# Optimization experiments

Hardware: AMD Instinct MI355X
Metric: run time of the kernel (lower is better)

The kernel has to match this reference:

```python
import jax, jax.numpy as jnp
import numpy as np

B, M, D, H, C = 256, 512, 768, 8, 768


def setup_inputs() -> dict:
    key = jax.random.key(0)
    ks = jax.random.split(key, 12)
    rn = lambda k, shp, s=1.0: jax.random.normal(k, shp, dtype=jnp.float32) * s
    w = 1.0 / np.sqrt(D)
    return dict(
        controller_state=rn(ks[0], (B, C)),
        write_data=rn(ks[1], (B, D)),
        memory=rn(ks[2], (M, D), 0.1),
        in_proj_w=rn(ks[3], (3 * D, D), w), in_proj_b=jnp.zeros((3 * D,), jnp.float32),
        out_w=rn(ks[4], (D, D), w), out_b=jnp.zeros((D,), jnp.float32),
        read_w=rn(ks[5], (D, C), w), read_b=jnp.zeros((D,), jnp.float32),
        write_w=rn(ks[6], (D, C), w), write_b=jnp.zeros((D,), jnp.float32),
        erase_w=rn(ks[7], (D, C), w), erase_b=jnp.zeros((D,), jnp.float32),
        ug_w=rn(ks[8], (1, C + D), w), ug_b=jnp.zeros((1,), jnp.float32),
        fg_w=rn(ks[9], (1, C + D), w), fg_b=jnp.zeros((1,), jnp.float32),
    )


def _mha(q, kv, in_proj_w, in_proj_b, out_w, out_b, num_heads):
    # q: [B,1,D] query, kv: [B,M,D] keys=values. Matches torch.nn.MultiheadAttention
    # (batch_first, eval mode -> no dropout, average_attn_weights=True).
    b, m, d = kv.shape
    dh = d // num_heads
    wq, wk, wv = jnp.split(in_proj_w, 3, axis=0)
    bq, bk, bv = jnp.split(in_proj_b, 3, axis=0)
    qh = (q @ wq.T + bq).reshape(b, 1, num_heads, dh).transpose(0, 2, 1, 3)   # [B,H,1,dh]
    kh = (kv @ wk.T + bk).reshape(b, m, num_heads, dh).transpose(0, 2, 1, 3)  # [B,H,M,dh]
    vh = (kv @ wv.T + bv).reshape(b, m, num_heads, dh).transpose(0, 2, 1, 3)
    scores = jnp.einsum('bhqd,bhkd->bhqk', qh, kh) / jnp.sqrt(jnp.float32(dh))
    attn = jax.nn.softmax(scores, axis=-1)                                    # [B,H,1,M]
    ctx = jnp.einsum('bhqk,bhkd->bhqd', attn, vh)
    ctx = ctx.transpose(0, 2, 1, 3).reshape(b, 1, d)
    out = ctx @ out_w.T + out_b
    return out, attn.mean(axis=1)  # out [B,1,D], weights averaged over heads [B,1,M]


def reference(controller_state, write_data, memory, in_proj_w, in_proj_b,
              out_w, out_b, read_w, read_b, write_w, write_b,
              erase_w, erase_b, ug_w, ug_b, fg_w, fg_b):
    b = controller_state.shape[0]
    memory_batch = jnp.broadcast_to(memory[None], (b,) + memory.shape)        # [B,M,D]

    read_key = (controller_state @ read_w.T + read_b)[:, None, :]             # [B,1,D]
    read_data, _ = _mha(read_key, memory_batch, in_proj_w, in_proj_b, out_w, out_b, H)
    read_data = read_data[:, 0, :]                                            # [B,D]

    write_key = (controller_state @ write_w.T + write_b)[:, None, :]
    erase_vec = jax.nn.sigmoid(controller_state @ erase_w.T + erase_b)[:, None, :]  # [B,1,D]
    _, write_weights = _mha(write_key, memory_batch, in_proj_w, in_proj_b, out_w, out_b, H)
    ww = write_weights[:, 0, :]                                               # [B,M]

    combined = jnp.concatenate([controller_state, read_data], axis=-1)        # [B,C+D]
    ug = jax.nn.sigmoid(combined @ ug_w.T + ug_b)                             # [B,1]
    fg = jax.nn.sigmoid(combined @ fg_w.T + fg_b)                             # [B,1]

    erase_term = ww[:, :, None] * erase_vec * fg[:, :, None]                  # [B,M,D]
    write_term = ww[:, :, None] * write_data[:, None, :] * ug[:, :, None]     # [B,M,D]
    updated_memory = memory_batch + (write_term - erase_term)
    return read_data, updated_memory
```

## Files before the change

kernel.cpp:

```cpp
#include <hip/hip_runtime.h>
#include <math.h>

#define B_ 256
#define M_ 512
#define D_ 768
#define H_ 8
#define DH_ 96
#define C_ 768

typedef float  f32x4_t __attribute__((ext_vector_type(4)));
typedef short  s16x8   __attribute__((ext_vector_type(8)));
typedef unsigned short u16;

__device__ __forceinline__ u16 cvt_bf16(float f) {
    union { float f; unsigned int u; } v; v.f = f;
    unsigned int r = (v.u + 0x7FFFu + ((v.u >> 16) & 1u)) >> 16;
    return (u16)r;
}
__device__ __forceinline__ float bf16_f32(u16 h) {
    union { unsigned int u; float f; } v; v.u = ((unsigned int)h) << 16;
    return v.f;
}

#define ACC_INIT {{0,0,0,0},{0,0,0,0},{0,0,0,0},{0,0,0,0}}
#define SCALE_ 0.10206207261596577f

template<int BK>
__device__ __forceinline__ void mm64b(
    const u16* __restrict__ A, int lda, const u16* __restrict__ B, int ldb,
    int ksteps, int bRowClamp, u16* lA, u16* lB, f32x4_t* acc, int nfrag)
{
    constexpr int NL = BK / 32;
    const int t = threadIdx.x;
    const int srow = t >> 2, kq = t & 3;
    const int l = t & 63, w = t >> 6;
    const int brow = srow < bRowClamp ? srow : bRowClamp;

    for (int ks = 0; ks < ksteps; ++ks) {
        s16x8 va[NL], vb[NL];
        #pragma unroll
        for (int c = 0; c < NL; ++c) {
            const int ko = ks * BK + (kq * NL + c) * 8;
            va[c] = *reinterpret_cast<const s16x8*>(A + (size_t)srow * lda + ko);
            vb[c] = *reinterpret_cast<const s16x8*>(B + (size_t)brow * ldb + ko);
        }
        __syncthreads();
        #pragma unroll
        for (int c = 0; c < NL; ++c) {
            const int kb = kq * NL + c;
            *reinterpret_cast<s16x8*>(lA + (kb * 64 + srow) * 8) = va[c];
            *reinterpret_cast<s16x8*>(lB + (kb * 64 + srow) * 8) = vb[c];
        }
        __syncthreads();
        #pragma unroll
        for (int ksub = 0; ksub < NL; ++ksub) {
            const int kb = (l >> 4) + ksub * 4;
            s16x8 af = *reinterpret_cast<const s16x8*>(lA + (kb * 64 + w * 16 + (l & 15)) * 8);
            #pragma unroll
            for (int nb = 0; nb < 4; ++nb) {
                if (nb < nfrag) {
                    s16x8 bf = *reinterpret_cast<const s16x8*>(lB + (kb * 64 + nb * 16 + (l & 15)) * 8);
                    acc[nb] = __builtin_amdgcn_mfma_f32_16x16x32_bf16(af, bf, acc[nb], 0, 0, 0);
                }
            }
        }
    }
}

__device__ __forceinline__ void epilogue_f32(
    const f32x4_t* acc, float* out, int ldo, int m0, int n0,
    const float* bias, int act, int nfrag)
{
    const int t = threadIdx.x, l = t & 63, w = t >> 6;
    const int mbase = m0 + w * 16 + (l >> 4) * 4;
    #pragma unroll
    for (int nb = 0; nb < 4; ++nb) {
        if (nb >= nfrag) break;
        const int col = n0 + nb * 16 + (l & 15);
        const float bv = bias ? bias[col] : 0.0f;
        #pragma unroll
        for (int r = 0; r < 4; ++r) {
            float v = acc[nb][r] + bv;
            if (act) v = 1.0f / (1.0f + expf(-v));
            out[(size_t)(mbase + r) * ldo + col] = v;
        }
    }
}

__device__ __forceinline__ void epilogue_bf16(
    const f32x4_t* acc, u16* out, int ldo, int m0, int n0,
    const float* bias, int nfrag)
{
    const int t = threadIdx.x, l = t & 63, w = t >> 6;
    const int mbase = m0 + w * 16 + (l >> 4) * 4;
    #pragma unroll
    for (int nb = 0; nb < 4; ++nb) {
        if (nb >= nfrag) break;
        const int col = n0 + nb * 16 + (l & 15);
        const float bv = bias ? bias[col] : 0.0f;
        #pragma unroll
        for (int r = 0; r < 4; ++r)
            out[(size_t)(mbase + r) * ldo + col] = cvt_bf16(acc[nb][r] + bv);
    }
}

__global__ __launch_bounds__(256) void conv_kernel(
    const float* __restrict__ mem, const float* __restrict__ cs,
    const float* __restrict__ ipw, const float* __restrict__ rw,
    const float* __restrict__ www, const float* __restrict__ ew,
    const float* __restrict__ outw, const float* __restrict__ outb,
    const float* __restrict__ ugw, const float* __restrict__ ugb,
    const float* __restrict__ fgw, const float* __restrict__ fgb,
    u16* __restrict__ memb, u16* __restrict__ csb, u16* __restrict__ ipwb,
    u16* __restrict__ rwb, u16* __restrict__ wwwb, u16* __restrict__ ewb,
    u16* __restrict__ outwb, float* __restrict__ vg, float* __restrict__ gc)
{
    __shared__ float sred[256];
    const int bid = blockIdx.x, t = threadIdx.x;

    if (bid < 2304) {
        const float* src; u16* dst; int base;
        if      (bid < 192)  { src = mem;  dst = memb;  base = bid; }
        else if (bid < 288)  { src = cs;   dst = csb;   base = bid - 192; }
        else if (bid < 1152) { src = ipw;  dst = ipwb;  base = bid - 288; }
        else if (bid < 1440) { src = rw;   dst = rwb;   base = bid - 1152; }
        else if (bid < 1728) { src = www;  dst = wwwb;  base = bid - 1440; }
        else if (bid < 2016) { src = ew;   dst = ewb;   base = bid - 1728; }
        else                 { src = outw; dst = outwb; base = bid - 2016; }
        const size_t i = ((size_t)base * 256 + t) * 8;
        float4 x = *reinterpret_cast<const float4*>(src + i);
        float4 y = *reinterpret_cast<const float4*>(src + i + 4);
        s16x8 o;
        o[0]=cvt_bf16(x.x); o[1]=cvt_bf16(x.y); o[2]=cvt_bf16(x.z); o[3]=cvt_bf16(x.w);
        o[4]=cvt_bf16(y.x); o[5]=cvt_bf16(y.y); o[6]=cvt_bf16(y.z); o[7]=cvt_bf16(y.w);
        *reinterpret_cast<s16x8*>(dst + i) = o;
    } else {
        const int lid = bid - 2304;
        const int v = lid / 12, kt = lid % 12;
        const float* gw = v == 0 ? ugw : fgw;
        const int c = t & 63, g = t >> 6;
        const int col = kt * 64 + c;
        float acc = 0.f;
        #pragma unroll 4
        for (int i = 0; i < 192; ++i) {
            const int row = g * 192 + i;
            acc += outw[(size_t)row * 768 + col] * gw[768 + row];
        }
        sred[t] = acc;
        __syncthreads();
        if (g == 0)
            vg[v * 768 + col] = sred[c] + sred[64 + c] + sred[128 + c] + sred[192 + c];
        if (kt == 0) {
            __syncthreads();
            float cp = outb[t] * gw[768 + t] + outb[t + 256] * gw[768 + t + 256]
                     + outb[t + 512] * gw[768 + t + 512];
            sred[t] = cp; __syncthreads();
            #pragma unroll
            for (int off = 128; off > 0; off >>= 1) {
                if (t < off) sred[t] += sred[t + off];
                __syncthreads();
            }
            if (t == 0) gc[v] = sred[0] + (v == 0 ? ugb[0] : fgb[0]);
        }
    }
}

__global__ __launch_bounds__(256) void stage1_kernel(
    const u16* __restrict__ memb, const u16* __restrict__ csb,
    const u16* __restrict__ ipwb, const float* __restrict__ ipb,
    const u16* __restrict__ rwb, const float* __restrict__ rb,
    const u16* __restrict__ wwwb, const float* __restrict__ ww_b,
    const u16* __restrict__ ewb, const float* __restrict__ eb,
    u16* __restrict__ khb, u16* __restrict__ vhT,
    u16* __restrict__ rwkeysb, float* __restrict__ erase)
{
    __shared__ u16 lA[8192], lB[8192];
    f32x4_t acc[4] = ACC_INIT;
    const int bid = blockIdx.x;
    if (bid < 192) {
        const int mt = bid / 24, nt = bid % 24;
        mm64b<64>(memb + (size_t)mt * 64 * 768, 768,
                  ipwb + (size_t)768 * 768 + (size_t)nt * 64 * 768, 768,
                  12, 63, lA, lB, acc, 4);
        const int t = threadIdx.x, l = t & 63, w = t >> 6;
        const int mbase = mt * 64 + w * 16 + (l >> 4) * 4;
        if (nt < 12) {
            #pragma unroll
            for (int nb = 0; nb < 4; ++nb) {
                const int col = nt * 64 + nb * 16 + (l & 15);
                const float bv = ipb[768 + col];
                #pragma unroll
                for (int r = 0; r < 4; ++r)
                    khb[(size_t)(mbase + r) * 768 + col] = cvt_bf16(acc[nb][r] + bv);
            }
        } else {
            #pragma unroll
            for (int nb = 0; nb < 4; ++nb) {
                const int cg = (nt - 12) * 64 + nb * 16 + (l & 15);
                const int h = cg / 96, d = cg % 96;
                const float bv = ipb[1536 + cg];
                u16* dst = vhT + ((size_t)h * 96 + d) * 512;
                #pragma unroll
                for (int r = 0; r < 4; ++r)
                    dst[mbase + r] = cvt_bf16(acc[nb][r] + bv);
            }
        }
    } else if (bid < 240) {
        const int lid = bid - 192, mt = lid / 12, nt = lid % 12;
        mm64b<64>(csb + (size_t)mt * 64 * 768, 768, rwb + (size_t)nt * 64 * 768, 768,
                  12, 63, lA, lB, acc, 4);
        epilogue_bf16(acc, rwkeysb, 768, mt * 64, nt * 64, rb, 4);
    } else if (bid < 288) {
        const int lid = bid - 240, mt = lid / 12, nt = lid % 12;
        mm64b<64>(csb + (size_t)mt * 64 * 768, 768, wwwb + (size_t)nt * 64 * 768, 768,
                  12, 63, lA, lB, acc, 4);
        epilogue_bf16(acc, rwkeysb + (size_t)256 * 768, 768, mt * 64, nt * 64, ww_b, 4);
    } else {
        const int lid = bid - 288, mt = lid / 12, nt = lid % 12;
        mm64b<64>(csb + (size_t)mt * 64 * 768, 768, ewb + (size_t)nt * 64 * 768, 768,
                  12, 63, lA, lB, acc, 4);
        epilogue_f32(acc, erase, 768, mt * 64, nt * 64, eb, 1, 4);
    }
}

__global__ __launch_bounds__(256) void stage2_kernel(
    const u16* __restrict__ rwkeysb, const u16* __restrict__ ipwb,
    const float* __restrict__ ipb, u16* __restrict__ qrwb)
{
    __shared__ u16 lA[8192], lB[8192];
    f32x4_t acc[4] = ACC_INIT;
    const int mt = blockIdx.x / 12, nt = blockIdx.x % 12;
    mm64b<64>(rwkeysb + (size_t)mt * 64 * 768, 768, ipwb + (size_t)nt * 64 * 768, 768,
              12, 63, lA, lB, acc, 4);
    epilogue_bf16(acc, qrwb, 768, mt * 64, nt * 64, ipb, 4);
}

__global__ __launch_bounds__(256) void scores_kernel(
    const u16* __restrict__ qrwb, const u16* __restrict__ khb, u16* __restrict__ E)
{
    __shared__ u16 lA[2048], lB[2048];
    f32x4_t acc[4] = ACC_INIT;
    const int h = blockIdx.y;
    const int mt = blockIdx.x >> 3, nt = blockIdx.x & 7;
    mm64b<32>(qrwb + (size_t)mt * 64 * 768 + h * 96, 768,
              khb + (size_t)nt * 64 * 768 + h * 96, 768, 3, 63, lA, lB, acc, 4);
    const int t = threadIdx.x, l = t & 63, w = t >> 6;
    const int mbase = mt * 64 + w * 16 + (l >> 4) * 4;
    #pragma unroll
    for (int nb = 0; nb < 4; ++nb) {
        const int col = nt * 64 + nb * 16 + (l & 15);
        #pragma unroll
        for (int r = 0; r < 4; ++r) {
            const float e = expf(fminf(acc[nb][r] * SCALE_, 30.0f));
            E[((size_t)h * 512 + mbase + r) * 512 + col] = cvt_bf16(e);
        }
    }
}

__global__ __launch_bounds__(256) void pv_kernel(
    const u16* __restrict__ E, const u16* __restrict__ vhT, u16* __restrict__ ctxb)
{
    __shared__ u16 lA[8192], lB[8192];
    __shared__ float rinv[64];
    f32x4_t acc[4] = ACC_INIT;
    const int h = blockIdx.z, mt = blockIdx.x, nt = blockIdx.y;
    const int n0 = nt * 64;
    const int nfrag = nt == 0 ? 4 : 2;
    const int bclamp = nt == 0 ? 63 : 31;

    const u16* A  = E + ((size_t)h * 512 + mt * 64) * 512;
    const u16* Bv = vhT + ((size_t)h * 96 + n0) * 512;

    const int t = threadIdx.x;
    const int srow = t >> 2, kq = t & 3;
    const int l = t & 63, w = t >> 6;
    const int brow = srow < bclamp ? srow : bclamp;

    float rs = 0.f;
    for (int ks = 0; ks < 8; ++ks) {
        s16x8 va[2], vb[2];
        #pragma unroll
        for (int c = 0; c < 2; ++c) {
            const int ko = ks * 64 + (kq * 2 + c) * 8;
            va[c] = *reinterpret_cast<const s16x8*>(A + (size_t)srow * 512 + ko);
            vb[c] = *reinterpret_cast<const s16x8*>(Bv + (size_t)brow * 512 + ko);
        }
        #pragma unroll
        for (int c = 0; c < 2; ++c)
            #pragma unroll
            for (int j = 0; j < 8; ++j)
                rs += bf16_f32((u16)va[c][j]);
        __syncthreads();
        #pragma unroll
        for (int c = 0; c < 2; ++c) {
            const int kb = kq * 2 + c;
            *reinterpret_cast<s16x8*>(lA + (kb * 64 + srow) * 8) = va[c];
            *reinterpret_cast<s16x8*>(lB + (kb * 64 + srow) * 8) = vb[c];
        }
        __syncthreads();
        #pragma unroll
        for (int ksub = 0; ksub < 2; ++ksub) {
            const int kb = (l >> 4) + ksub * 4;
            s16x8 af = *reinterpret_cast<const s16x8*>(lA + (kb * 64 + w * 16 + (l & 15)) * 8);
            #pragma unroll
            for (int nb = 0; nb < 4; ++nb) {
                if (nb < nfrag) {
                    s16x8 bf = *reinterpret_cast<const s16x8*>(lB + (kb * 64 + nb * 16 + (l & 15)) * 8);
                    acc[nb] = __builtin_amdgcn_mfma_f32_16x16x32_bf16(af, bf, acc[nb], 0, 0, 0);
                }
            }
        }
    }
    rs += __shfl_xor(rs, 1);
    rs += __shfl_xor(rs, 2);
    if (kq == 0) rinv[srow] = 1.0f / rs;
    __syncthreads();

    const int mbase = w * 16 + (l >> 4) * 4;
    #pragma unroll
    for (int nb = 0; nb < 4; ++nb) {
        if (nb >= nfrag) break;
        const int col = n0 + nb * 16 + (l & 15);
        #pragma unroll
        for (int r = 0; r < 4; ++r) {
            const float v = acc[nb][r] * rinv[mbase + r];
            ctxb[(size_t)(mt * 64 + mbase + r) * 768 + h * 96 + col] = cvt_bf16(v);
        }
    }
}

__global__ __launch_bounds__(256) void finalize_kernel(
    const u16* __restrict__ ctxb, const u16* __restrict__ outwb,
    const float* __restrict__ outb, float* __restrict__ rd_out,
    const float* __restrict__ cs, const float* __restrict__ wdta,
    const float* __restrict__ erase,
    const float* __restrict__ ugw, const float* __restrict__ fgw,
    const float* __restrict__ vg, const float* __restrict__ gc,
    const u16* __restrict__ E,
    float* __restrict__ delta, float* __restrict__ wwb)
{
    __shared__ u16 lA[8192], lB[8192];
    const int bid = blockIdx.x, t = threadIdx.x;
    if (bid < 48) {
        f32x4_t acc[4] = ACC_INIT;
        const int mt = bid / 12, nt = bid % 12;
        mm64b<64>(ctxb + (size_t)mt * 64 * 768, 768, outwb + (size_t)nt * 64 * 768, 768,
                  12, 63, lA, lB, acc, 4);
        epilogue_f32(acc, rd_out, 768, mt * 64, nt * 64, outb, 0, 4);
    } else if (bid < 304) {
        const int b = bid - 48;
        __shared__ float red[8];
        float pu = 0.f, pf = 0.f;
        #pragma unroll
        for (int c = 0; c < 3; ++c) {
            const int i = t + c * 256;
            const float cv = cs[(size_t)b * 768 + i];
            const float xv = bf16_f32(ctxb[(size_t)b * 768 + i]);
            pu += cv * ugw[i] + xv * vg[i];
            pf += cv * fgw[i] + xv * vg[768 + i];
        }
        const int w = t >> 6, l = t & 63;
        #pragma unroll
        for (int off = 32; off > 0; off >>= 1) {
            pu += __shfl_xor(pu, off);
            pf += __shfl_xor(pf, off);
        }
        if (l == 0) { red[w] = pu; red[4 + w] = pf; }
        __syncthreads();
        const float ug = 1.0f / (1.0f + expf(-(red[0] + red[1] + red[2] + red[3] + gc[0])));
        const float fg = 1.0f / (1.0f + expf(-(red[4] + red[5] + red[6] + red[7] + gc[1])));
        #pragma unroll
        for (int c = 0; c < 3; ++c) {
            const int i = t + c * 256;
            delta[(size_t)b * 768 + i] = wdta[(size_t)b * 768 + i] * ug
                                       - erase[(size_t)b * 768 + i] * fg;
        }
    } else {
        const int b = bid - 304;
        __shared__ float linv8[8];
        const int w = t >> 6, l = t & 63;
        #pragma unroll
        for (int hh = 0; hh < 2; ++hh) {
            const int h = w * 2 + hh;
            const u16* row = E + ((size_t)h * 512 + 256 + b) * 512;
            float s = 0.f;
            #pragma unroll
            for (int c = 0; c < 8; ++c) s += bf16_f32(row[c * 64 + l]);
            #pragma unroll
            for (int off = 32; off > 0; off >>= 1) s += __shfl_xor(s, off);
            if (l == 0) linv8[h] = 1.0f / s;
        }
        __syncthreads();
        #pragma unroll
        for (int mm_ = 0; mm_ < 2; ++mm_) {
            const int m = t + mm_ * 256;
            float s = 0.f;
            #pragma unroll
            for (int h = 0; h < H_; ++h)
                s += bf16_f32(E[((size_t)h * 512 + 256 + b) * 512 + m]) * linv8[h];
            wwb[(size_t)b * 512 + m] = s * 0.125f;
        }
    }
}

__global__ __launch_bounds__(192) void update_mem(
    const float* __restrict__ mem, const float* __restrict__ ww,
    const float* __restrict__ delta, float* __restrict__ out)
{
    const int blk = blockIdx.x;
    const int b   = blk >> 6;
    const int m0  = (blk & 63) << 3;
    const int t   = threadIdx.x;

    const f32x4_t d4 = *reinterpret_cast<const f32x4_t*>(delta + (size_t)b * D_ + t * 4);
    const f32x4_t* m4 = reinterpret_cast<const f32x4_t*>(mem);
    f32x4_t* o4 = reinterpret_cast<f32x4_t*>(out + (size_t)b * M_ * D_);

    #pragma unroll
    for (int i = 0; i < 8; ++i) {
        const int m = m0 + i;
        const float w = ww[(size_t)b * M_ + m];
        f32x4_t mm = m4[(size_t)m * 192 + t];
        f32x4_t r = mm + w * d4;
        __builtin_nontemporal_store(r, &o4[(size_t)m * 192 + t]);
    }
}

extern "C" void kernel_launch(void* const* d_in, const int* in_sizes, int n_in,
                              void* d_out, int out_size, void* d_ws, size_t ws_size,
                              hipStream_t stream)
{
    const float* cs   = (const float*)d_in[0];
    const float* wdta = (const float*)d_in[1];
    const float* mem  = (const float*)d_in[2];
    const float* ipw  = (const float*)d_in[3];
    const float* ipb  = (const float*)d_in[4];
    const float* outw = (const float*)d_in[5];
    const float* outb = (const float*)d_in[6];
    const float* rw   = (const float*)d_in[7];
    const float* rb   = (const float*)d_in[8];
    const float* ww_w = (const float*)d_in[9];
    const float* ww_b = (const float*)d_in[10];
    const float* ew   = (const float*)d_in[11];
    const float* eb   = (const float*)d_in[12];
    const float* ugw  = (const float*)d_in[13];
    const float* ugb  = (const float*)d_in[14];
    const float* fgw  = (const float*)d_in[15];
    const float* fgb  = (const float*)d_in[16];

    float* rd_out  = (float*)d_out;
    float* mem_out = (float*)d_out + B_ * D_;

    float* S0 = mem_out;
    u16*   memb    = (u16*)(S0 + 0);
    u16*   csb     = (u16*)(S0 + 196608);
    u16*   ipwb    = (u16*)(S0 + 294912);
    u16*   rwb     = (u16*)(S0 + 1179648);
    u16*   wwwb    = (u16*)(S0 + 1474560);
    u16*   ewb     = (u16*)(S0 + 1769472);
    u16*   outwb   = (u16*)(S0 + 2064384);
    u16*   khb     = (u16*)(S0 + 2359296);
    u16*   vhT     = (u16*)(S0 + 2555904);
    u16*   rwkeysb = (u16*)(S0 + 2752512);
    u16*   qrwb    = (u16*)(S0 + 2949120);

    float* ws    = (float*)d_ws;
    float* erase = ws;
    u16*   ctxb  = (u16*)(ws + 196608);
    u16*   E     = (u16*)(ws + 294912);
    float* vg    =        ws + 1343488;
    float* gc    =        ws + 1345024;
    float* delta =        ws + 1345040;
    float* wwb   =        ws + 1541648;

    conv_kernel<<<2328, 256, 0, stream>>>(mem, cs, ipw, rw, ww_w, ew, outw, outb,
                                          ugw, ugb, fgw, fgb,
                                          memb, csb, ipwb, rwb, wwwb, ewb, outwb,
                                          vg, gc);
    stage1_kernel<<<336, 256, 0, stream>>>(memb, csb, ipwb, ipb, rwb, rb, wwwb, ww_b,
                                           ewb, eb, khb, vhT, rwkeysb, erase);
    stage2_kernel<<<96, 256, 0, stream>>>(rwkeysb, ipwb, ipb, qrwb);
    scores_kernel<<<dim3(64, 8), 256, 0, stream>>>(qrwb, khb, E);
    pv_kernel<<<dim3(4, 2, 8), 256, 0, stream>>>(E, vhT, ctxb);
    finalize_kernel<<<560, 256, 0, stream>>>(ctxb, outwb, outb, rd_out,
                                             cs, wdta, erase, ugw, fgw, vg, gc,
                                             E, delta, wwb);
    update_mem<<<B_ * (M_ / 8), 192, 0, stream>>>(mem, wwb, delta, mem_out);
}
```

Before: 149.9 us.

## Fuse all stages into a persistent cooperative megakernel with grid syncs

Replaces the seven separate kernel launches with one cooperative kernel of 512 persistent blocks. Each stage is now a device function, and the stages are separated by grid-wide syncs. The aim is to remove launch gaps and inter-kernel idle time. The memory-update stage is also reworked to loop over 256-thread blocks with 6 float4 items per thread. In exchange, the streaming update runs at a fixed, lower occupancy, and every grid.sync adds barrier cost. If the cooperative launch fails, the code falls back to separate launches.

```diff
diff --git a/kernel.cpp b/kernel.cpp
--- a/kernel.cpp
+++ b/kernel.cpp
@@ -1,5 +1,8 @@
 #include <hip/hip_runtime.h>
+#include <hip/hip_cooperative_groups.h>
 #include <math.h>
+
+namespace cg = cooperative_groups;
 
 #define B_ 256
 #define M_ 512
@@ -24,6 +27,14 @@
 
 #define ACC_INIT {{0,0,0,0},{0,0,0,0},{0,0,0,0},{0,0,0,0}}
 #define SCALE_ 0.10206207261596577f
+
+struct P {
+    const float *cs, *wdta, *mem, *ipw, *ipb, *outw, *outb;
+    const float *rw, *rb, *www_w, *www_b, *ew, *eb, *ugw, *ugb, *fgw, *fgb;
+    u16 *memb, *csb, *ipwb, *rwb, *wwwb, *ewb, *outwb;
+    u16 *khb, *vhT, *rwkeysb, *qrwb, *E, *ctxb;
+    float *erase, *vg, *gc, *delta, *wwb, *rd_out, *mem_out;
+};
 
 template<int BK>
 __device__ __forceinline__ void mm64b(
@@ -104,29 +115,18 @@
     }
 }
 
-__global__ __launch_bounds__(256) void conv_kernel(
-    const float* __restrict__ mem, const float* __restrict__ cs,
-    const float* __restrict__ ipw, const float* __restrict__ rw,
-    const float* __restrict__ www, const float* __restrict__ ew,
-    const float* __restrict__ outw, const float* __restrict__ outb,
-    const float* __restrict__ ugw, const float* __restrict__ ugb,
-    const float* __restrict__ fgw, const float* __restrict__ fgb,
-    u16* __restrict__ memb, u16* __restrict__ csb, u16* __restrict__ ipwb,
-    u16* __restrict__ rwb, u16* __restrict__ wwwb, u16* __restrict__ ewb,
-    u16* __restrict__ outwb, float* __restrict__ vg, float* __restrict__ gc)
-{
-    __shared__ float sred[256];
-    const int bid = blockIdx.x, t = threadIdx.x;
-
+
+__device__ __forceinline__ void conv_body(const P& p, int bid, int t, float* sred)
+{
     if (bid < 2304) {
         const float* src; u16* dst; int base;
-        if      (bid < 192)  { src = mem;  dst = memb;  base = bid; }
-        else if (bid < 288)  { src = cs;   dst = csb;   base = bid - 192; }
-        else if (bid < 1152) { src = ipw;  dst = ipwb;  base = bid - 288; }
-        else if (bid < 1440) { src = rw;   dst = rwb;   base = bid - 1152; }
-        else if (bid < 1728) { src = www;  dst = wwwb;  base = bid - 1440; }
-        else if (bid < 2016) { src = ew;   dst = ewb;   base = bid - 1728; }
-        else                 { src = outw; dst = outwb; base = bid - 2016; }
+        if      (bid < 192)  { src = p.mem;   dst = p.memb;  base = bid; }
+        else if (bid < 288)  { src = p.cs;    dst = p.csb;   base = bid - 192; }
+        else if (bid < 1152) { src = p.ipw;   dst = p.ipwb;  base = bid - 288; }
+        else if (bid < 1440) { src = p.rw;    dst = p.rwb;   base = bid - 1152; }
+        else if (bid < 1728) { src = p.www_w; dst = p.wwwb;  base = bid - 1440; }
+        else if (bid < 2016) { src = p.ew;    dst = p.ewb;   base = bid - 1728; }
+        else                 { src = p.outw;  dst = p.outwb; base = bid - 2016; }
         const size_t i = ((size_t)base * 256 + t) * 8;
         float4 x = *reinterpret_cast<const float4*>(src + i);
         float4 y = *reinterpret_cast<const float4*>(src + i + 4);
@@ -137,50 +137,42 @@
     } else {
         const int lid = bid - 2304;
         const int v = lid / 12, kt = lid % 12;
-        const float* gw = v == 0 ? ugw : fgw;
+        const float* gw = v == 0 ? p.ugw : p.fgw;
         const int c = t & 63, g = t >> 6;
         const int col = kt * 64 + c;
         float acc = 0.f;
         #pragma unroll 4
         for (int i = 0; i < 192; ++i) {
             const int row = g * 192 + i;
-            acc += outw[(size_t)row * 768 + col] * gw[768 + row];
+            acc += p.outw[(size_t)row * 768 + col] * gw[768 + row];
         }
         sred[t] = acc;
         __syncthreads();
         if (g == 0)
-            vg[v * 768 + col] = sred[c] + sred[64 + c] + sred[128 + c] + sred[192 + c];
+            p.vg[v * 768 + col] = sred[c] + sred[64 + c] + sred[128 + c] + sred[192 + c];
         if (kt == 0) {
             __syncthreads();
-            float cp = outb[t] * gw[768 + t] + outb[t + 256] * gw[768 + t + 256]
-                     + outb[t + 512] * gw[768 + t + 512];
+            float cp = p.outb[t] * gw[768 + t] + p.outb[t + 256] * gw[768 + t + 256]
+                     + p.outb[t + 512] * gw[768 + t + 512];
             sred[t] = cp; __syncthreads();
             #pragma unroll
             for (int off = 128; off > 0; off >>= 1) {
                 if (t < off) sred[t] += sred[t + off];
                 __syncthreads();
             }
-            if (t == 0) gc[v] = sred[0] + (v == 0 ? ugb[0] : fgb[0]);
-        }
-    }
-}
-
-__global__ __launch_bounds__(256) void stage1_kernel(
-    const u16* __restrict__ memb, const u16* __restrict__ csb,
-    const u16* __restrict__ ipwb, const float* __restrict__ ipb,
-    const u16* __restrict__ rwb, const float* __restrict__ rb,
-    const u16* __restrict__ wwwb, const float* __restrict__ ww_b,
-    const u16* __restrict__ ewb, const float* __restrict__ eb,
-    u16* __restrict__ khb, u16* __restrict__ vhT,
-    u16* __restrict__ rwkeysb, float* __restrict__ erase)
-{
-    __shared__ u16 lA[8192], lB[8192];
+            if (t == 0) p.gc[v] = sred[0] + (v == 0 ? p.ugb[0] : p.fgb[0]);
+        }
+        __syncthreads();
+    }
+}
+
+__device__ __forceinline__ void stage1_body(const P& p, int bid, u16* lA, u16* lB)
+{
     f32x4_t acc[4] = ACC_INIT;
-    const int bid = blockIdx.x;
     if (bid < 192) {
         const int mt = bid / 24, nt = bid % 24;
-        mm64b<64>(memb + (size_t)mt * 64 * 768, 768,
-                  ipwb + (size_t)768 * 768 + (size_t)nt * 64 * 768, 768,
+        mm64b<64>(p.memb + (size_t)mt * 64 * 768, 768,
+                  p.ipwb + (size_t)768 * 768 + (size_t)nt * 64 * 768, 768,
                   12, 63, lA, lB, acc, 4);
         const int t = threadIdx.x, l = t & 63, w = t >> 6;
         const int mbase = mt * 64 + w * 16 + (l >> 4) * 4;
@@ -188,18 +180,18 @@
             #pragma unroll
             for (int nb = 0; nb < 4; ++nb) {
                 const int col = nt * 64 + nb * 16 + (l & 15);
-                const float bv = ipb[768 + col];
+                const float bv = p.ipb[768 + col];
                 #pragma unroll
                 for (int r = 0; r < 4; ++r)
-                    khb[(size_t)(mbase + r) * 768 + col] = cvt_bf16(acc[nb][r] + bv);
+                    p.khb[(size_t)(mbase + r) * 768 + col] = cvt_bf16(acc[nb][r] + bv);
             }
         } else {
             #pragma unroll
             for (int nb = 0; nb < 4; ++nb) {
                 const int cg = (nt - 12) * 64 + nb * 16 + (l & 15);
                 const int h = cg / 96, d = cg % 96;
-                const float bv = ipb[1536 + cg];
-                u16* dst = vhT + ((size_t)h * 96 + d) * 512;
+                const float bv = p.ipb[1536 + cg];
+                u16* dst = p.vhT + ((size_t)h * 96 + d) * 512;
                 #pragma unroll
                 for (int r = 0; r < 4; ++r)
                     dst[mbase + r] = cvt_bf16(acc[nb][r] + bv);
@@ -207,43 +199,39 @@
         }
     } else if (bid < 240) {
         const int lid = bid - 192, mt = lid / 12, nt = lid % 12;
-        mm64b<64>(csb + (size_t)mt * 64 * 768, 768, rwb + (size_t)nt * 64 * 768, 768,
+        mm64b<64>(p.csb + (size_t)mt * 64 * 768, 768, p.rwb + (size_t)nt * 64 * 768, 768,
                   12, 63, lA, lB, acc, 4);
-        epilogue_bf16(acc, rwkeysb, 768, mt * 64, nt * 64, rb, 4);
+        epilogue_bf16(acc, p.rwkeysb, 768, mt * 64, nt * 64, p.rb, 4);
     } else if (bid < 288) {
         const int lid = bid - 240, mt = lid / 12, nt = lid % 12;
-        mm64b<64>(csb + (size_t)mt * 64 * 768, 768, wwwb + (size_t)nt * 64 * 768, 768,
+        mm64b<64>(p.csb + (size_t)mt * 64 * 768, 768, p.wwwb + (size_t)nt * 64 * 768, 768,
                   12, 63, lA, lB, acc, 4);
-        epilogue_bf16(acc, rwkeysb + (size_t)256 * 768, 768, mt * 64, nt * 64, ww_b, 4);
+        epilogue_bf16(acc, p.rwkeysb + (size_t)256 * 768, 768, mt * 64, nt * 64, p.www_b, 4);
     } else {
         const int lid = bid - 288, mt = lid / 12, nt = lid % 12;
-        mm64b<64>(csb + (size_t)mt * 64 * 768, 768, ewb + (size_t)nt * 64 * 768, 768,
+        mm64b<64>(p.csb + (size_t)mt * 64 * 768, 768, p.ewb + (size_t)nt * 64 * 768, 768,
                   12, 63, lA, lB, acc, 4);
-        epilogue_f32(acc, erase, 768, mt * 64, nt * 64, eb, 1, 4);
-    }
-}
-
-__global__ __launch_bounds__(256) void stage2_kernel(
-    const u16* __restrict__ rwkeysb, const u16* __restrict__ ipwb,
-    const float* __restrict__ ipb, u16* __restrict__ qrwb)
-{
-    __shared__ u16 lA[8192], lB[8192];
+        epilogue_f32(acc, p.erase, 768, mt * 64, nt * 64, p.eb, 1, 4);
+    }
+}
+
+__device__ __forceinline__ void stage2_body(const P& p, int bid, u16* lA, u16* lB)
+{
     f32x4_t acc[4] = ACC_INIT;
-    const int mt = blockIdx.x / 12, nt = blockIdx.x % 12;
-    mm64b<64>(rwkeysb + (size_t)mt * 64 * 768, 768, ipwb + (size_t)nt * 64 * 768, 768,
+    const int mt = bid / 12, nt = bid % 12;
+    mm64b<64>(p.rwkeysb + (size_t)mt * 64 * 768, 768, p.ipwb + (size_t)nt * 64 * 768, 768,
               12, 63, lA, lB, acc, 4);
-    epilogue_bf16(acc, qrwb, 768, mt * 64, nt * 64, ipb, 4);
-}
-
-__global__ __launch_bounds__(256) void scores_kernel(
-    const u16* __restrict__ qrwb, const u16* __restrict__ khb, u16* __restrict__ E)
-{
-    __shared__ u16 lA[2048], lB[2048];
+    epilogue_bf16(acc, p.qrwb, 768, mt * 64, nt * 64, p.ipb, 4);
+}
+
+__device__ __forceinline__ void scores_body(const P& p, int bid, u16* lA, u16* lB)
+{
     f32x4_t acc[4] = ACC_INIT;
-    const int h = blockIdx.y;
-    const int mt = blockIdx.x >> 3, nt = blockIdx.x & 7;
-    mm64b<32>(qrwb + (size_t)mt * 64 * 768 + h * 96, 768,
-              khb + (size_t)nt * 64 * 768 + h * 96, 768, 3, 63, lA, lB, acc, 4);
+    const int h = bid >> 6;
+    const int x = bid & 63;
+    const int mt = x >> 3, nt = x & 7;
+    mm64b<32>(p.qrwb + (size_t)mt * 64 * 768 + h * 96, 768,
+              p.khb + (size_t)nt * 64 * 768 + h * 96, 768, 3, 63, lA, lB, acc, 4);
     const int t = threadIdx.x, l = t & 63, w = t >> 6;
     const int mbase = mt * 64 + w * 16 + (l >> 4) * 4;
     #pragma unroll
@@ -252,24 +240,23 @@
         #pragma unroll
         for (int r = 0; r < 4; ++r) {
             const float e = expf(fminf(acc[nb][r] * SCALE_, 30.0f));
-            E[((size_t)h * 512 + mbase + r) * 512 + col] = cvt_bf16(e);
-        }
-    }
-}
-
-__global__ __launch_bounds__(256) void pv_kernel(
-    const u16* __restrict__ E, const u16* __restrict__ vhT, u16* __restrict__ ctxb)
-{
-    __shared__ u16 lA[8192], lB[8192];
-    __shared__ float rinv[64];
+            p.E[((size_t)h * 512 + mbase + r) * 512 + col] = cvt_bf16(e);
+        }
+    }
+}
+
+__device__ __forceinline__ void pv_body(const P& p, int bid, u16* lA, u16* lB, float* rinv)
+{
     f32x4_t acc[4] = ACC_INIT;
-    const int h = blockIdx.z, mt = blockIdx.x, nt = blockIdx.y;
+    const int h = bid >> 3;
+    const int x = bid & 7;
+    const int mt = x >> 1, nt = x & 1;
     const int n0 = nt * 64;
     const int nfrag = nt == 0 ? 4 : 2;
     const int bclamp = nt == 0 ? 63 : 31;
 
-    const u16* A  = E + ((size_t)h * 512 + mt * 64) * 512;
-    const u16* Bv = vhT + ((size_t)h * 96 + n0) * 512;
+    const u16* A  = p.E + ((size_t)h * 512 + mt * 64) * 512;
+    const u16* Bv = p.vhT + ((size_t)h * 96 + n0) * 512;
 
     const int t = threadIdx.x;
     const int srow = t >> 2, kq = t & 3;
@@ -324,40 +311,31 @@
         #pragma unroll
         for (int r = 0; r < 4; ++r) {
             const float v = acc[nb][r] * rinv[mbase + r];
-            ctxb[(size_t)(mt * 64 + mbase + r) * 768 + h * 96 + col] = cvt_bf16(v);
-        }
-    }
-}
-
-__global__ __launch_bounds__(256) void finalize_kernel(
-    const u16* __restrict__ ctxb, const u16* __restrict__ outwb,
-    const float* __restrict__ outb, float* __restrict__ rd_out,
-    const float* __restrict__ cs, const float* __restrict__ wdta,
-    const float* __restrict__ erase,
-    const float* __restrict__ ugw, const float* __restrict__ fgw,
-    const float* __restrict__ vg, const float* __restrict__ gc,
-    const u16* __restrict__ E,
-    float* __restrict__ delta, float* __restrict__ wwb)
-{
-    __shared__ u16 lA[8192], lB[8192];
-    const int bid = blockIdx.x, t = threadIdx.x;
+            p.ctxb[(size_t)(mt * 64 + mbase + r) * 768 + h * 96 + col] = cvt_bf16(v);
+        }
+    }
+    __syncthreads();
+}
+
+__device__ __forceinline__ void finalize_body(const P& p, int bid, int t,
+                                              u16* lA, u16* lB, float* red8, float* linv8)
+{
     if (bid < 48) {
         f32x4_t acc[4] = ACC_INIT;
         const int mt = bid / 12, nt = bid % 12;
-        mm64b<64>(ctxb + (size_t)mt * 64 * 768, 768, outwb + (size_t)nt * 64 * 768, 768,
+        mm64b<64>(p.ctxb + (size_t)mt * 64 * 768, 768, p.outwb + (size_t)nt * 64 * 768, 768,
                   12, 63, lA, lB, acc, 4);
-        epilogue_f32(acc, rd_out, 768, mt * 64, nt * 64, outb, 0, 4);
+        epilogue_f32(acc, p.rd_out, 768, mt * 64, nt * 64, p.outb, 0, 4);
     } else if (bid < 304) {
         const int b = bid - 48;
-        __shared__ float red[8];
         float pu = 0.f, pf = 0.f;
         #pragma unroll
         for (int c = 0; c < 3; ++c) {
             const int i = t + c * 256;
-            const float cv = cs[(size_t)b * 768 + i];
-            const float xv = bf16_f32(ctxb[(size_t)b * 768 + i]);
-            pu += cv * ugw[i] + xv * vg[i];
-            pf += cv * fgw[i] + xv * vg[768 + i];
+            const float cv = p.cs[(size_t)b * 768 + i];
+            const float xv = bf16_f32(p.ctxb[(size_t)b * 768 + i]);
+            pu += cv * p.ugw[i] + xv * p.vg[i];
+            pf += cv * p.fgw[i] + xv * p.vg[768 + i];
         }
         const int w = t >> 6, l = t & 63;
         #pragma unroll
@@ -365,24 +343,24 @@
             pu += __shfl_xor(pu, off);
             pf += __shfl_xor(pf, off);
         }
-        if (l == 0) { red[w] = pu; red[4 + w] = pf; }
-        __syncthreads();
-        const float ug = 1.0f / (1.0f + expf(-(red[0] + red[1] + red[2] + red[3] + gc[0])));
-        const float fg = 1.0f / (1.0f + expf(-(red[4] + red[5] + red[6] + red[7] + gc[1])));
+        if (l == 0) { red8[w] = pu; red8[4 + w] = pf; }
+        __syncthreads();
+        const float ug = 1.0f / (1.0f + expf(-(red8[0] + red8[1] + red8[2] + red8[3] + p.gc[0])));
+        const float fg = 1.0f / (1.0f + expf(-(red8[4] + red8[5] + red8[6] + red8[7] + p.gc[1])));
         #pragma unroll
         for (int c = 0; c < 3; ++c) {
             const int i = t + c * 256;
-            delta[(size_t)b * 768 + i] = wdta[(size_t)b * 768 + i] * ug
-                                       - erase[(size_t)b * 768 + i] * fg;
-        }
+            p.delta[(size_t)b * 768 + i] = p.wdta[(size_t)b * 768 + i] * ug
+                                         - p.erase[(size_t)b * 768 + i] * fg;
+        }
+        __syncthreads();
     } else {
         const int b = bid - 304;
-        __shared__ float linv8[8];
         const int w = t >> 6, l = t & 63;
         #pragma unroll
         for (int hh = 0; hh < 2; ++hh) {
             const int h = w * 2 + hh;
-            const u16* row = E + ((size_t)h * 512 + 256 + b) * 512;
+            const u16* row = p.E + ((size_t)h * 512 + 256 + b) * 512;
             float s = 0.f;
             #pragma unroll
             for (int c = 0; c < 8; ++c) s += bf16_f32(row[c * 64 + l]);
@@ -397,93 +375,147 @@
             float s = 0.f;
             #pragma unroll
             for (int h = 0; h < H_; ++h)
-                s += bf16_f32(E[((size_t)h * 512 + 256 + b) * 512 + m]) * linv8[h];
-            wwb[(size_t)b * 512 + m] = s * 0.125f;
-        }
-    }
-}
-
-__global__ __launch_bounds__(192) void update_mem(
-    const float* __restrict__ mem, const float* __restrict__ ww,
-    const float* __restrict__ delta, float* __restrict__ out)
-{
-    const int blk = blockIdx.x;
-    const int b   = blk >> 6;
-    const int m0  = (blk & 63) << 3;
-    const int t   = threadIdx.x;
-
-    const f32x4_t d4 = *reinterpret_cast<const f32x4_t*>(delta + (size_t)b * D_ + t * 4);
-    const f32x4_t* m4 = reinterpret_cast<const f32x4_t*>(mem);
-    f32x4_t* o4 = reinterpret_cast<f32x4_t*>(out + (size_t)b * M_ * D_);
-
+                s += bf16_f32(p.E[((size_t)h * 512 + 256 + b) * 512 + m]) * linv8[h];
+            p.wwb[(size_t)b * 512 + m] = s * 0.125f;
+        }
+        __syncthreads();
+    }
+}
+
+__device__ __forceinline__ void update_body(const P& p, int u, int t)
+{
+    const int b  = u >> 6;
+    const int m0 = (u & 63) << 3;
+    const f32x4_t* m4 = reinterpret_cast<const f32x4_t*>(p.mem);
+    f32x4_t* o4 = reinterpret_cast<f32x4_t*>(p.mem_out + (size_t)b * 393216);
+    const float* drow = p.delta + (size_t)b * 768;
     #pragma unroll
-    for (int i = 0; i < 8; ++i) {
-        const int m = m0 + i;
-        const float w = ww[(size_t)b * M_ + m];
-        f32x4_t mm = m4[(size_t)m * 192 + t];
-        f32x4_t r = mm + w * d4;
-        __builtin_nontemporal_store(r, &o4[(size_t)m * 192 + t]);
-    }
+    for (int ph = 0; ph < 6; ++ph) {
+        const int c = t + ph * 256;
+        const int m = m0 + c / 192;
+        const int d4 = c % 192;
+        const float w = p.wwb[(size_t)b * 512 + m];
+        const f32x4_t dd = *reinterpret_cast<const f32x4_t*>(drow + d4 * 4);
+        f32x4_t mm = m4[(size_t)m * 192 + d4];
+        f32x4_t r = mm + w * dd;
+        __builtin_nontemporal_store(r, &o4[(size_t)m * 192 + d4]);
+    }
+}
+
+__global__ __launch_bounds__(256, 2) void mega_kernel(P p)
+{
+    cg::grid_group grid = cg::this_grid();
+    __shared__ u16 lA[8192], lB[8192];
+    __shared__ float sred[256];
+    __shared__ float rinv[64];
+    __shared__ float red8[8];
+    __shared__ float linv8[8];
+    const int bid = blockIdx.x, t = threadIdx.x;
+
+    for (int u = bid; u < 2328; u += 512) conv_body(p, u, t, sred);
+    grid.sync();
+    if (bid < 336) stage1_body(p, bid, lA, lB);
+    grid.sync();
+    if (bid < 96) stage2_body(p, bid, lA, lB);
+    grid.sync();
+    scores_body(p, bid, lA, lB);
+    grid.sync();
+    if (bid < 64) pv_body(p, bid, lA, lB, rinv);
+    grid.sync();
+    for (int u = bid; u < 560; u += 512) finalize_body(p, u, t, lA, lB, red8, linv8);
+    grid.sync();
+    for (int u = bid; u < 16384; u += 512) update_body(p, u, t);
+}
+
+__global__ __launch_bounds__(256) void k_conv(P p) {
+    __shared__ float sred[256];
+    conv_body(p, blockIdx.x, threadIdx.x, sred);
+}
+__global__ __launch_bounds__(256) void k_stage1(P p) {
+    __shared__ u16 lA[8192], lB[8192];
+    stage1_body(p, blockIdx.x, lA, lB);
+}
+__global__ __launch_bounds__(256) void k_stage2(P p) {
+    __shared__ u16 lA[8192], lB[8192];
+    stage2_body(p, blockIdx.x, lA, lB);
+}
+__global__ __launch_bounds__(256) void k_scores(P p) {
+    __shared__ u16 lA[2048], lB[2048];
+    scores_body(p, blockIdx.x, lA, lB);
+}
+__global__ __launch_bounds__(256) void k_pv(P p) {
+    __shared__ u16 lA[8192], lB[8192];
+    __shared__ float rinv[64];
+    pv_body(p, blockIdx.x, lA, lB, rinv);
+}
+__global__ __launch_bounds__(256) void k_finalize(P p) {
+    __shared__ u16 lA[8192], lB[8192];
+    __shared__ float red8[8], linv8[8];
+    finalize_body(p, blockIdx.x, threadIdx.x, lA, lB, red8, linv8);
+}
+__global__ __launch_bounds__(256) void k_update(P p) {
+    update_body(p, blockIdx.x, threadIdx.x);
 }
 
 extern "C" void kernel_launch(void* const* d_in, const int* in_sizes, int n_in,
                               void* d_out, int out_size, void* d_ws, size_t ws_size,
                               hipStream_t stream)
 {
-    const float* cs   = (const float*)d_in[0];
-    const float* wdta = (const float*)d_in[1];
-    const float* mem  = (const float*)d_in[2];
-    const float* ipw  = (const float*)d_in[3];
-    const float* ipb  = (const float*)d_in[4];
-    const float* outw = (const float*)d_in[5];
-    const float* outb = (const float*)d_in[6];
-    const float* rw   = (const float*)d_in[7];
-    const float* rb   = (const float*)d_in[8];
-    const float* ww_w = (const float*)d_in[9];
-    const float* ww_b = (const float*)d_in[10];
-    const float* ew   = (const float*)d_in[11];
-    const float* eb   = (const float*)d_in[12];
-    const float* ugw  = (const float*)d_in[13];
-    const float* ugb  = (const float*)d_in[14];
-    const float* fgw  = (const float*)d_in[15];
-    const float* fgb  = (const float*)d_in[16];
-
-    float* rd_out  = (float*)d_out;
-    float* mem_out = (float*)d_out + B_ * D_;
-
-    float* S0 = mem_out;
-    u16*   memb    = (u16*)(S0 + 0);
-    u16*   csb     = (u16*)(S0 + 196608);
-    u16*   ipwb    = (u16*)(S0 + 294912);
-    u16*   rwb     = (u16*)(S0 + 1179648);
-    u16*   wwwb    = (u16*)(S0 + 1474560);
-    u16*   ewb     = (u16*)(S0 + 1769472);
-    u16*   outwb   = (u16*)(S0 + 2064384);
-    u16*   khb     = (u16*)(S0 + 2359296);
-    u16*   vhT     = (u16*)(S0 + 2555904);
-    u16*   rwkeysb = (u16*)(S0 + 2752512);
-    u16*   qrwb    = (u16*)(S0 + 2949120);
-
-    float* ws    = (float*)d_ws;
-    float* erase = ws;
-    u16*   ctxb  = (u16*)(ws + 196608);
-    u16*   E     = (u16*)(ws + 294912);
-    float* vg    =        ws + 1343488;
-    float* gc    =        ws + 1345024;
-    float* delta =        ws + 1345040;
-    float* wwb   =        ws + 1541648;
-
-    conv_kernel<<<2328, 256, 0, stream>>>(mem, cs, ipw, rw, ww_w, ew, outw, outb,
-                                          ugw, ugb, fgw, fgb,
-                                          memb, csb, ipwb, rwb, wwwb, ewb, outwb,
-                                          vg, gc);
-    stage1_kernel<<<336, 256, 0, stream>>>(memb, csb, ipwb, ipb, rwb, rb, wwwb, ww_b,
-                                           ewb, eb, khb, vhT, rwkeysb, erase);
-    stage2_kernel<<<96, 256, 0, stream>>>(rwkeysb, ipwb, ipb, qrwb);
-    scores_kernel<<<dim3(64, 8), 256, 0, stream>>>(qrwb, khb, E);
-    pv_kernel<<<dim3(4, 2, 8), 256, 0, stream>>>(E, vhT, ctxb);
-    finalize_kernel<<<560, 256, 0, stream>>>(ctxb, outwb, outb, rd_out,
-                                             cs, wdta, erase, ugw, fgw, vg, gc,
-                                             E, delta, wwb);
-    update_mem<<<B_ * (M_ / 8), 192, 0, stream>>>(mem, wwb, delta, mem_out);
-}
+    P p;
+    p.cs    = (const float*)d_in[0];
+    p.wdta  = (const float*)d_in[1];
+    p.mem   = (const float*)d_in[2];
+    p.ipw   = (const float*)d_in[3];
+    p.ipb   = (const float*)d_in[4];
+    p.outw  = (const float*)d_in[5];
+    p.outb  = (const float*)d_in[6];
+    p.rw    = (const float*)d_in[7];
+    p.rb    = (const float*)d_in[8];
+    p.www_w = (const float*)d_in[9];
+    p.www_b = (const float*)d_in[10];
+    p.ew    = (const float*)d_in[11];
+    p.eb    = (const float*)d_in[12];
+    p.ugw   = (const float*)d_in[13];
+    p.ugb   = (const float*)d_in[14];
+    p.fgw   = (const float*)d_in[15];
+    p.fgb   = (const float*)d_in[16];
+
+    p.rd_out  = (float*)d_out;
+    p.mem_out = (float*)d_out + B_ * D_;
+
+    float* S0 = p.mem_out;
+    p.memb    = (u16*)(S0 + 0);
+    p.csb     = (u16*)(S0 + 196608);
+    p.ipwb    = (u16*)(S0 + 294912);
+    p.rwb     = (u16*)(S0 + 1179648);
+    p.wwwb    = (u16*)(S0 + 1474560);
+    p.ewb     = (u16*)(S0 + 1769472);
+    p.outwb   = (u16*)(S0 + 2064384);
+    p.khb     = (u16*)(S0 + 2359296);
+    p.vhT     = (u16*)(S0 + 2555904);
+    p.rwkeysb = (u16*)(S0 + 2752512);
+    p.qrwb    = (u16*)(S0 + 2949120);
+
+    float* ws = (float*)d_ws;
+    p.erase = ws;
+    p.ctxb  = (u16*)(ws + 196608);
+    p.E     = (u16*)(ws + 294912);
+    p.vg    = ws + 1343488;
+    p.gc    = ws + 1345024;
+    p.delta = ws + 1345040;
+    p.wwb   = ws + 1541648;
+
+    void* args[] = { &p };
+    hipError_t err = hipLaunchCooperativeKernel((const void*)mega_kernel,
+                                                dim3(512), dim3(256), args, 0, stream);
+    if (err != hipSuccess) {
+        (void)hipGetLastError();
+        k_conv<<<2328, 256, 0, stream>>>(p);
+        k_stage1<<<336, 256, 0, stream>>>(p);
+        k_stage2<<<96, 256, 0, stream>>>(p);
+        k_scores<<<512, 256, 0, stream>>>(p);
+        k_pv<<<64, 256, 0, stream>>>(p);
+        k_finalize<<<560, 256, 0, stream>>>(p);
+        k_update<<<16384, 256, 0, stream>>>(p);
+    }
+}
```

Measured after the change: 493.0 us. 229% more time.

## Split gates/ww into own kernel and fuse out-projection GEMM with memory update

Applied to the files above, without the earlier changes.

The gate and write-weight computations move into a separate kernel, and the out-projection GEMM now runs in the same launch as the memory update. The memory update is reshaped to 256-thread blocks covering 8 rows each. The bf16 out-weight buffer moves from the output scratch region into the workspace, because the update now writes mem_out while the GEMM still reads outwb. This overlaps the small GEMM tail with the bandwidth-bound update, at the cost of extra div/mod indexing in the update path.

```diff
diff --git a/kernel.cpp b/kernel.cpp
--- a/kernel.cpp
+++ b/kernel.cpp
@@ -329,15 +329,77 @@
     }
 }
 
-__global__ __launch_bounds__(256) void finalize_kernel(
-    const u16* __restrict__ ctxb, const u16* __restrict__ outwb,
-    const float* __restrict__ outb, float* __restrict__ rd_out,
+__global__ __launch_bounds__(256) void gatesww_kernel(
+    const u16* __restrict__ ctxb,
     const float* __restrict__ cs, const float* __restrict__ wdta,
     const float* __restrict__ erase,
     const float* __restrict__ ugw, const float* __restrict__ fgw,
     const float* __restrict__ vg, const float* __restrict__ gc,
     const u16* __restrict__ E,
     float* __restrict__ delta, float* __restrict__ wwb)
+{
+    const int bid = blockIdx.x, t = threadIdx.x;
+    if (bid < 256) {
+        const int b = bid;
+        __shared__ float red[8];
+        float pu = 0.f, pf = 0.f;
+        #pragma unroll
+        for (int c = 0; c < 3; ++c) {
+            const int i = t + c * 256;
+            const float cv = cs[(size_t)b * 768 + i];
+            const float xv = bf16_f32(ctxb[(size_t)b * 768 + i]);
+            pu += cv * ugw[i] + xv * vg[i];
+            pf += cv * fgw[i] + xv * vg[768 + i];
+        }
+        const int w = t >> 6, l = t & 63;
+        #pragma unroll
+        for (int off = 32; off > 0; off >>= 1) {
+            pu += __shfl_xor(pu, off);
+            pf += __shfl_xor(pf, off);
+        }
+        if (l == 0) { red[w] = pu; red[4 + w] = pf; }
+        __syncthreads();
+        const float ug = 1.0f / (1.0f + expf(-(red[0] + red[1] + red[2] + red[3] + gc[0])));
+        const float fg = 1.0f / (1.0f + expf(-(red[4] + red[5] + red[6] + red[7] + gc[1])));
+        #pragma unroll
+        for (int c = 0; c < 3; ++c) {
+            const int i = t + c * 256;
+            delta[(size_t)b * 768 + i] = wdta[(size_t)b * 768 + i] * ug
+                                       - erase[(size_t)b * 768 + i] * fg;
+        }
+    } else {
+        const int b = bid - 256;
+        __shared__ float linv8[8];
+        const int w = t >> 6, l = t & 63;
+        #pragma unroll
+        for (int hh = 0; hh < 2; ++hh) {
+            const int h = w * 2 + hh;
+            const u16* row = E + ((size_t)h * 512 + 256 + b) * 512;
+            float s = 0.f;
+            #pragma unroll
+            for (int c = 0; c < 8; ++c) s += bf16_f32(row[c * 64 + l]);
+            #pragma unroll
+            for (int off = 32; off > 0; off >>= 1) s += __shfl_xor(s, off);
+            if (l == 0) linv8[h] = 1.0f / s;
+        }
+        __syncthreads();
+        #pragma unroll
+        for (int mm_ = 0; mm_ < 2; ++mm_) {
+            const int m = t + mm_ * 256;
+            float s = 0.f;
+            #pragma unroll
+            for (int h = 0; h < H_; ++h)
+                s += bf16_f32(E[((size_t)h * 512 + 256 + b) * 512 + m]) * linv8[h];
+            wwb[(size_t)b * 512 + m] = s * 0.125f;
+        }
+    }
+}
+
+__global__ __launch_bounds__(256) void final_kernel(
+    const u16* __restrict__ ctxb, const u16* __restrict__ outwb,
+    const float* __restrict__ outb, float* __restrict__ rd_out,
+    const float* __restrict__ mem, const float* __restrict__ wwb,
+    const float* __restrict__ delta, float* __restrict__ mem_out)
 {
     __shared__ u16 lA[8192], lB[8192];
     const int bid = blockIdx.x, t = threadIdx.x;
@@ -347,82 +409,24 @@
         mm64b<64>(ctxb + (size_t)mt * 64 * 768, 768, outwb + (size_t)nt * 64 * 768, 768,
                   12, 63, lA, lB, acc, 4);
         epilogue_f32(acc, rd_out, 768, mt * 64, nt * 64, outb, 0, 4);
-    } else if (bid < 304) {
-        const int b = bid - 48;
-        __shared__ float red[8];
-        float pu = 0.f, pf = 0.f;
-        #pragma unroll
-        for (int c = 0; c < 3; ++c) {
-            const int i = t + c * 256;
-            const float cv = cs[(size_t)b * 768 + i];
-            const float xv = bf16_f32(ctxb[(size_t)b * 768 + i]);
-            pu += cv * ugw[i] + xv * vg[i];
-            pf += cv * fgw[i] + xv * vg[768 + i];
-        }
-        const int w = t >> 6, l = t & 63;
-        #pragma unroll
-        for (int off = 32; off > 0; off >>= 1) {
-            pu += __shfl_xor(pu, off);
-            pf += __shfl_xor(pf, off);
-        }
-        if (l == 0) { red[w] = pu; red[4 + w] = pf; }
-        __syncthreads();
-        const float ug = 1.0f / (1.0f + expf(-(red[0] + red[1] + red[2] + red[3] + gc[0])));
-        const float fg = 1.0f / (1.0f + expf(-(red[4] + red[5] + red[6] + red[7] + gc[1])));
-        #pragma unroll
-        for (int c = 0; c < 3; ++c) {
-            const int i = t + c * 256;
-            delta[(size_t)b * 768 + i] = wdta[(size_t)b * 768 + i] * ug
-                                       - erase[(size_t)b * 768 + i] * fg;
-        }
     } else {
-        const int b = bid - 304;
-        __shared__ float linv8[8];
-        const int w = t >> 6, l = t & 63;
-        #pragma unroll
-        for (int hh = 0; hh < 2; ++hh) {
-            const int h = w * 2 + hh;
-            const u16* row = E + ((size_t)h * 512 + 256 + b) * 512;
-            float s = 0.f;
-            #pragma unroll
-            for (int c = 0; c < 8; ++c) s += bf16_f32(row[c * 64 + l]);
-            #pragma unroll
-            for (int off = 32; off > 0; off >>= 1) s += __shfl_xor(s, off);
-            if (l == 0) linv8[h] = 1.0f / s;
-        }
-        __syncthreads();
-        #pragma unroll
-        for (int mm_ = 0; mm_ < 2; ++mm_) {
-            const int m = t + mm_ * 256;
-            float s = 0.f;
-            #pragma unroll
-            for (int h = 0; h < H_; ++h)
-                s += bf16_f32(E[((size_t)h * 512 + 256 + b) * 512 + m]) * linv8[h];
-            wwb[(size_t)b * 512 + m] = s * 0.125f;
-        }
-    }
-}
-
-__global__ __launch_bounds__(192) void update_mem(
-    const float* __restrict__ mem, const float* __restrict__ ww,
-    const float* __restrict__ delta, float* __restrict__ out)
-{
-    const int blk = blockIdx.x;
-    const int b   = blk >> 6;
-    const int m0  = (blk & 63) << 3;
-    const int t   = threadIdx.x;
-
-    const f32x4_t d4 = *reinterpret_cast<const f32x4_t*>(delta + (size_t)b * D_ + t * 4);
-    const f32x4_t* m4 = reinterpret_cast<const f32x4_t*>(mem);
-    f32x4_t* o4 = reinterpret_cast<f32x4_t*>(out + (size_t)b * M_ * D_);
-
-    #pragma unroll
-    for (int i = 0; i < 8; ++i) {
-        const int m = m0 + i;
-        const float w = ww[(size_t)b * M_ + m];
-        f32x4_t mm = m4[(size_t)m * 192 + t];
-        f32x4_t r = mm + w * d4;
-        __builtin_nontemporal_store(r, &o4[(size_t)m * 192 + t]);
+        const int u = bid - 48;
+        const int b  = u >> 6;
+        const int m0 = (u & 63) << 3;
+        const f32x4_t* m4 = reinterpret_cast<const f32x4_t*>(mem);
+        f32x4_t* o4 = reinterpret_cast<f32x4_t*>(mem_out + (size_t)b * 393216);
+        const float* drow = delta + (size_t)b * 768;
+        #pragma unroll
+        for (int ph = 0; ph < 6; ++ph) {
+            const int c = t + ph * 256;
+            const int m = m0 + c / 192;
+            const int d4 = c % 192;
+            const float w = wwb[(size_t)b * 512 + m];
+            const f32x4_t dd = *reinterpret_cast<const f32x4_t*>(drow + d4 * 4);
+            f32x4_t mm = m4[(size_t)m * 192 + d4];
+            f32x4_t r = mm + w * dd;
+            __builtin_nontemporal_store(r, &o4[(size_t)m * 192 + d4]);
+        }
     }
 }
 
@@ -458,11 +462,10 @@
     u16*   rwb     = (u16*)(S0 + 1179648);
     u16*   wwwb    = (u16*)(S0 + 1474560);
     u16*   ewb     = (u16*)(S0 + 1769472);
-    u16*   outwb   = (u16*)(S0 + 2064384);
-    u16*   khb     = (u16*)(S0 + 2359296);
-    u16*   vhT     = (u16*)(S0 + 2555904);
-    u16*   rwkeysb = (u16*)(S0 + 2752512);
-    u16*   qrwb    = (u16*)(S0 + 2949120);
+    u16*   khb     = (u16*)(S0 + 2064384);
+    u16*   vhT     = (u16*)(S0 + 2260992);
+    u16*   rwkeysb = (u16*)(S0 + 2457600);
+    u16*   qrwb    = (u16*)(S0 + 2654208);
 
     float* ws    = (float*)d_ws;
     float* erase = ws;
@@ -472,6 +475,7 @@
     float* gc    =        ws + 1345024;
     float* delta =        ws + 1345040;
     float* wwb   =        ws + 1541648;
+    u16*   outwb = (u16*)(ws + 1672720);
 
     conv_kernel<<<2328, 256, 0, stream>>>(mem, cs, ipw, rw, ww_w, ew, outw, outb,
                                           ugw, ugb, fgw, fgb,
@@ -482,8 +486,8 @@
     stage2_kernel<<<96, 256, 0, stream>>>(rwkeysb, ipwb, ipb, qrwb);
     scores_kernel<<<dim3(64, 8), 256, 0, stream>>>(qrwb, khb, E);
     pv_kernel<<<dim3(4, 2, 8), 256, 0, stream>>>(E, vhT, ctxb);
-    finalize_kernel<<<560, 256, 0, stream>>>(ctxb, outwb, outb, rd_out,
-                                             cs, wdta, erase, ugw, fgw, vg, gc,
-                                             E, delta, wwb);
-    update_mem<<<B_ * (M_ / 8), 192, 0, stream>>>(mem, wwb, delta, mem_out);
-}
+    gatesww_kernel<<<512, 256, 0, stream>>>(ctxb, cs, wdta, erase, ugw, fgw, vg, gc,
+                                            E, delta, wwb);
+    final_kernel<<<16432, 256, 0, stream>>>(ctxb, outwb, outb, rd_out,
+                                            mem, wwb, delta, mem_out);
+}
```

Result: faster. 141.1 us (-5.8%).
